# Performance work log

Hardware: AMD Instinct MI355X
Metric: run time of the kernel (lower is better)

The kernel has to match this reference:

```python
import jax, jax.numpy as jnp
import numpy as np

L, K, C, D, E = 4, 3, 512, 512, 512   # layers, kwidth, channels, embed_dim, encoding_dim
T, B, S, V, MAXT = 1024, 16, 512, 32, 1024


def setup_inputs() -> dict:
    key = jax.random.key(0)
    ks = jax.random.split(key, 16)
    n = lambda k, sh, s=0.02: jax.random.normal(k, sh, dtype=jnp.float32) * s
    return {
        "labels": jax.random.randint(ks[0], (T, B), 0, V),
        "enc_seq": jax.random.uniform(ks[1], (S, B, E), dtype=jnp.float32),
        "label_embed_W": n(ks[2], (V, D)),
        "time_embed_W": n(ks[3], (MAXT, D)),
        "conv_glu_w": n(ks[4], (L, C, C, K)),
        "conv_glu_b": jnp.zeros((L, C), jnp.float32),
        "conv_id_w": n(ks[5], (L, C, C, K)),
        "conv_id_b": jnp.zeros((L, C), jnp.float32),
        "res_proj_w": n(ks[6], (L, C, C)),
        "res_proj_b": jnp.zeros((L, C), jnp.float32),
        "inres_w": n(ks[7], (L, C, D)),
        "inres_b": jnp.zeros((L, C), jnp.float32),
        "in2enc_w": n(ks[8], (L, E, C)),
        "in2enc_b": jnp.ones((L, E), jnp.float32),  # positive bias keeps sum-normalizer well conditioned
        "lab2enc_w": n(ks[9], (L, E, D)),
        "lab2enc_b": jnp.zeros((L, E), jnp.float32),
        "enc2in_w": n(ks[10], (L, C, E)),
        "enc2in_b": jnp.zeros((L, C), jnp.float32),
        "out_res_w": n(ks[11], (V, D)),
        "out_res_b": jnp.zeros((V,), jnp.float32),
        "out_proj_w": n(ks[12], (V, C)),
        "out_proj_b": jnp.zeros((V,), jnp.float32),
    }


def causal_conv(x, w, b):
    # x: (T, B, Cin); w: (Cout, Cin, K) -> left-padded (causal) conv, out (T, B, Cout)
    x_ = jnp.transpose(x, (1, 2, 0))  # (B, Cin, T)
    y = jax.lax.conv_general_dilated(
        x_, w, window_strides=(1,), padding=[(w.shape[-1] - 1, 0)],
        dimension_numbers=("NCH", "OIH", "NCH"))
    return jnp.transpose(y, (2, 0, 1)) + b


def reference(labels, enc_seq, label_embed_W, time_embed_W, conv_glu_w, conv_glu_b,
              conv_id_w, conv_id_b, res_proj_w, res_proj_b, inres_w, inres_b,
              in2enc_w, in2enc_b, lab2enc_w, lab2enc_b, enc2in_w, enc2in_b,
              out_res_w, out_res_b, out_proj_w, out_proj_b):
    Tn = labels.shape[0]
    emb = label_embed_W[labels] + time_embed_W[jnp.arange(Tn)][:, None, :]  # (T,B,D)
    h = emb
    for i in range(conv_glu_w.shape[0]):
        x = causal_conv(h, conv_glu_w[i], conv_glu_b[i])
        g = causal_conv(h, conv_id_w[i], conv_id_b[i])
        conv_out = (x * jax.nn.sigmoid(g)
                    + jnp.einsum('tbc,oc->tbo', h, res_proj_w[i]) + res_proj_b[i])
        # attention: dot-product scores normalized by their SUM over encoder axis (no softmax)
        d = (jnp.einsum('tbc,ec->tbe', conv_out, in2enc_w[i]) + in2enc_b[i]
             + jnp.einsum('tbd,ed->tbe', emb, lab2enc_w[i]) + lab2enc_b[i])
        raw = jnp.einsum('tbe,sbe->tsb', d, enc_seq)          # (T,S,B)
        attn = raw / jnp.sum(raw, axis=1, keepdims=True)
        ctx = jnp.einsum('tsb,sbe->tbe', attn, enc_seq)        # (T,B,E)
        ctx_proj = jnp.einsum('tbe,ce->tbc', ctx, enc2in_w[i]) + enc2in_b[i]
        h = conv_out + ctx_proj + jnp.einsum('tbd,cd->tbc', emb, inres_w[i]) + inres_b[i]
    out = (jnp.einsum('tbc,vc->tbv', h, out_proj_w) + out_proj_b
           + jnp.einsum('tbd,vd->tbv', emb, out_res_w) + out_res_b)
    return out
```

## Files before the change

### kernel.cpp

```cpp
#include <hip/hip_runtime.h>
#include <math.h>

#define Tn 1024
#define Bn 16
#define Sn 512
#define Vn 32
#define Cn 512
#define En 512
#define Ln 4
#define Kw 3
#define MROWS 16384
#define PADROWS 32
#define PADE (PADROWS * Cn)

typedef short bf16x8 __attribute__((ext_vector_type(8)));
typedef float f32x4 __attribute__((ext_vector_type(4)));

__device__ __forceinline__ unsigned short cvt_bf16(float x) {
  unsigned u = __builtin_bit_cast(unsigned, x);
  u = (u + 0x7FFFu + ((u >> 16) & 1u)) >> 16;
  return (unsigned short)u;
}
__device__ __forceinline__ float bf2f(unsigned short h) {
  unsigned u = ((unsigned)h) << 16;
  return __builtin_bit_cast(float, u);
}

#define GL16(g, l)                                                                     \
  __builtin_amdgcn_global_load_lds((const __attribute__((address_space(1))) void*)(g), \
                                   (__attribute__((address_space(3))) void*)(l), 16, 0, 0)

template <int N>
__device__ __forceinline__ void wait_vm_bar() {
  asm volatile("s_waitcnt vmcnt(%0)\n\ts_barrier" ::"i"(N) : "memory");
}
__device__ __forceinline__ void tail_bar() {
  asm volatile("s_waitcnt lgkmcnt(0)\n\ts_barrier" ::: "memory");
}

__device__ __forceinline__ const unsigned short* seg_sel(const unsigned short* s0,
                                                         const unsigned short* s1,
                                                         const unsigned short* s2, int q) {
  const unsigned short* r = s0;
  r = (q == 1) ? s1 : r;
  r = (q == 2) ? s2 : r;
  return r;
}

template <int EPI, int NKT>
__global__ __launch_bounds__(512, 4) void g2(
    const unsigned short* __restrict__ a0, const unsigned short* __restrict__ a1,
    const unsigned short* __restrict__ a2, int ald, size_t az,
    const unsigned short* __restrict__ b0, const unsigned short* __restrict__ b1,
    const unsigned short* __restrict__ b2, int bld, size_t bz,
    const float* __restrict__ bias, const unsigned short* __restrict__ addbf,
    const float* __restrict__ dden, unsigned short* __restrict__ out, int old_, size_t oz) {
  __shared__ char SA[32768], SB[32768];
  const int tid = threadIdx.x;
  const int lane = tid & 63, wave = tid >> 6;
  const int r15 = lane & 15;
  const int sq = ((lane >> 4) ^ ((r15 >> 1) & 3)) << 4;
  const int waveM = (wave >> 2) << 6;
  const int waveN = (wave & 3) << 5;
  const int m0 = blockIdx.x * 128, n0 = blockIdx.y * 128;
  const int z = blockIdx.z;
  const unsigned short* A0 = a0 + (size_t)z * az;
  const unsigned short* A1 = a1 + (size_t)z * az;
  const unsigned short* A2 = a2 + (size_t)z * az;
  const unsigned short* B0 = b0 + (size_t)z * bz;
  const unsigned short* B1 = b1 + (size_t)z * bz;
  const unsigned short* B2 = b2 + (size_t)z * bz;
  const int strow = tid >> 2;
  const int stcol = ((tid & 3) ^ ((tid >> 3) & 3)) << 3;
  const int lofs = tid * 16;
  f32x4 acc[4][2] = {};

#define STAGE_T(KT, SL)                                                                  \
  do {                                                                                   \
    const unsigned short* ab_ = seg_sel(A0, A1, A2, (KT) >> 3) +                         \
                                (size_t)(m0 + strow) * ald + (((KT) & 7) << 6) + stcol;  \
    const unsigned short* bb_ = seg_sel(B0, B1, B2, (KT) >> 3) +                         \
                                (size_t)(n0 + strow) * bld + (((KT) & 7) << 6) + stcol;  \
    GL16(ab_, SA + (SL) * 16384 + lofs);                                                 \
    GL16(ab_ + 32, SA + (SL) * 16384 + 8192 + lofs);                                     \
    GL16(bb_, SB + (SL) * 16384 + lofs);                                                 \
    GL16(bb_ + 32, SB + (SL) * 16384 + 8192 + lofs);                                     \
  } while (0)

  STAGE_T(0, 0);
  for (int kt = 0; kt < NKT; ++kt) {
    const int sl = kt & 1;
    if (kt + 1 < NKT) {
      STAGE_T(kt + 1, sl ^ 1);
      wait_vm_bar<4>();
    } else {
      wait_vm_bar<0>();
    }
    const char* abase = SA + sl * 16384 + (waveM + r15) * 64 + sq;
    const char* bbase = SB + sl * 16384 + (waveN + r15) * 64 + sq;
    __builtin_amdgcn_s_setprio(1);
#pragma unroll
    for (int kp = 0; kp < 2; ++kp) {
      bf16x8 af[4], bfv[2];
#pragma unroll
      for (int i = 0; i < 4; ++i) af[i] = *(const bf16x8*)(abase + kp * 8192 + i * 1024);
#pragma unroll
      for (int j = 0; j < 2; ++j) bfv[j] = *(const bf16x8*)(bbase + kp * 8192 + j * 1024);
#pragma unroll
      for (int i = 0; i < 4; ++i)
#pragma unroll
        for (int j = 0; j < 2; ++j)
          acc[i][j] = __builtin_amdgcn_mfma_f32_16x16x32_bf16(af[i], bfv[j], acc[i][j], 0, 0, 0);
    }
    __builtin_amdgcn_s_setprio(0);
    tail_bar();
  }
#undef STAGE_T

  const int q4 = (lane >> 4) << 2;
#pragma unroll
  for (int i = 0; i < 4; ++i) {
    int row = m0 + waveM + i * 16 + q4;
    if constexpr (EPI == 0) {
      int xcol = ((n0 + waveN) >> 1) + r15;
      float bx = bias[n0 + waveN + r15];
      float bg = bias[n0 + waveN + 16 + r15];
#pragma unroll
      for (int rr = 0; rr < 4; ++rr) {
        float xv = acc[i][0][rr] + bx;
        float gv = acc[i][1][rr] + bg;
        float sg = 1.f / (1.f + __expf(-gv));
        out[(size_t)(row + rr) * 512 + xcol] = cvt_bf16(xv * sg);
      }
    } else if constexpr (EPI == 3) {
#pragma unroll
      for (int rr = 0; rr < 4; ++rr) {
        float inv = 1.f / dden[z + (size_t)(row + rr) * 16];
#pragma unroll
        for (int j = 0; j < 2; ++j) {
          int col = n0 + waveN + j * 16 + r15;
          out[(size_t)z * oz + (size_t)(row + rr) * old_ + col] = cvt_bf16(acc[i][j][rr] * inv);
        }
      }
    } else {
#pragma unroll
      for (int j = 0; j < 2; ++j) {
        int col = n0 + waveN + j * 16 + r15;
        float bb = (EPI == 4) ? 0.f : bias[col];
#pragma unroll
        for (int rr = 0; rr < 4; ++rr) {
          size_t o = (size_t)z * oz + (size_t)(row + rr) * old_ + col;
          float v = acc[i][j][rr] + bb;
          if constexpr (EPI == 2) v += bf2f(addbf[o]);
          out[o] = cvt_bf16(v);
        }
      }
    }
  }
}

__global__ __launch_bounds__(256, 4) void k_outm(const unsigned short* __restrict__ hd,
                                                 const unsigned short* __restrict__ embd,
                                                 const unsigned short* __restrict__ wcat2,
                                                 const float* __restrict__ bcat2,
                                                 float* __restrict__ out) {
  __shared__ char SA[32768];
  __shared__ char SBo[8192];
  const int tid = threadIdx.x;
  const int lane = tid & 63, wave = tid >> 6;
  const int r15 = lane & 15;
  const int sq = ((lane >> 4) ^ ((r15 >> 1) & 3)) << 4;
  const int waveM = wave << 5;
  const int m0 = blockIdx.x * 128;
  f32x4 acc[2][2] = {};
  const int aru = ((tid & 255) + 0);
  (void)aru;

#define OSTAGE(KT, SL)                                                                         \
  do {                                                                                         \
    const unsigned short* aseg = ((KT) < 8) ? hd : embd;                                       \
    int kc = ((KT) & 7) << 6;                                                                  \
    _Pragma("unroll") for (int q = 0; q < 2; ++q) {                                            \
      int unit = q * 256 + tid;                                                                \
      int row = unit >> 2, chunk = unit & 3;                                                   \
      int swc = chunk ^ ((row >> 1) & 3);                                                      \
      GL16(aseg + (size_t)(m0 + row) * 512 + kc + swc * 8, SA + (SL) * 16384 + unit * 16);     \
      GL16(aseg + (size_t)(m0 + row) * 512 + kc + 32 + swc * 8,                                \
           SA + (SL) * 16384 + 8192 + unit * 16);                                              \
    }                                                                                          \
    {                                                                                          \
      int half = tid >> 7;                                                                     \
      int u = tid & 127;                                                                       \
      int row = u >> 2, chunk = u & 3;                                                         \
      int swc = chunk ^ ((row >> 1) & 3);                                                      \
      GL16(wcat2 + (size_t)row * 1024 + ((KT) << 6) + half * 32 + swc * 8,                     \
           SBo + (SL) * 4096 + half * 2048 + u * 16);                                          \
    }                                                                                          \
  } while (0)

  OSTAGE(0, 0);
  for (int kt = 0; kt < 16; ++kt) {
    const int sl = kt & 1;
    if (kt + 1 < 16) {
      OSTAGE(kt + 1, sl ^ 1);
      wait_vm_bar<5>();
    } else {
      wait_vm_bar<0>();
    }
    const char* abase = SA + sl * 16384 + (waveM + r15) * 64 + sq;
    const char* bbase = SBo + sl * 4096 + r15 * 64 + sq;
    __builtin_amdgcn_s_setprio(1);
#pragma unroll
    for (int kp = 0; kp < 2; ++kp) {
      bf16x8 af[2], bfv[2];
#pragma unroll
      for (int i = 0; i < 2; ++i) af[i] = *(const bf16x8*)(abase + kp * 8192 + i * 1024);
#pragma unroll
      for (int j = 0; j < 2; ++j) bfv[j] = *(const bf16x8*)(bbase + kp * 2048 + j * 1024);
#pragma unroll
      for (int i = 0; i < 2; ++i)
#pragma unroll
        for (int j = 0; j < 2; ++j)
          acc[i][j] = __builtin_amdgcn_mfma_f32_16x16x32_bf16(af[i], bfv[j], acc[i][j], 0, 0, 0);
    }
    __builtin_amdgcn_s_setprio(0);
    tail_bar();
  }
#undef OSTAGE

  const int q4 = (lane >> 4) << 2;
#pragma unroll
  for (int i = 0; i < 2; ++i) {
    int row = m0 + waveM + i * 16 + q4;
#pragma unroll
    for (int j = 0; j < 2; ++j) {
      int col = j * 16 + r15;
      float bb = bcat2[col];
#pragma unroll
      for (int rr = 0; rr < 4; ++rr)
        out[(size_t)(row + rr) * 32 + col] = acc[i][j][rr] + bb;
    }
  }
}


__global__ __launch_bounds__(256) void emb_kernel(const int* __restrict__ labels,
                                                  const float* __restrict__ labW,
                                                  const float* __restrict__ timeW,
                                                  unsigned short* __restrict__ embd) {
  int idx = blockIdx.x * 256 + threadIdx.x;
  int dd = idx & 511;
  int m = idx >> 9;
  int t = m >> 4;
  embd[idx] = cvt_bf16(labW[labels[m] * 512 + dd] + timeW[t * 512 + dd]);
}

__global__ void k_zeropad(unsigned short* a, unsigned short* b, unsigned short* c) {
  int i = blockIdx.x * 256 + threadIdx.x;
  a[i] = 0; b[i] = 0; c[i] = 0;
}

__global__ void k_wcat(const float* __restrict__ wx, const float* __restrict__ wg,
                       unsigned short* __restrict__ wcat) {
  int idx = blockIdx.x * 256 + threadIdx.x;
  int k = idx % 1536;
  int tmp = idx / 1536;
  int orow = tmp & 1023;
  int l = tmp >> 10;
  int tap = k >> 9, c = k & 511;
  int q = orow >> 5, r = orow & 31;
  int srow = q * 16 + (r & 15);
  const float* src = (r < 16) ? wx : wg;
  float v = src[(((size_t)l * 512 + srow) * 512 + c) * 3 + tap];
  wcat[idx] = cvt_bf16(v);
}

__global__ void k_biascat(const float* __restrict__ bx, const float* __restrict__ bg,
                          float* __restrict__ bcat) {
  int idx = blockIdx.x * 256 + threadIdx.x;
  int orow = idx & 1023, l = idx >> 10;
  int q = orow >> 5, r = orow & 31;
  bcat[idx] = (r < 16) ? bx[l * 512 + q * 16 + r] : bg[l * 512 + q * 16 + (r & 15)];
}

__global__ void k_wcat2(const float* __restrict__ opw, const float* __restrict__ orw,
                        const float* __restrict__ opb, const float* __restrict__ orb,
                        unsigned short* __restrict__ wcat2, float* __restrict__ bcat2) {
  int idx = blockIdx.x * 256 + threadIdx.x;
  int v = idx >> 10, k = idx & 1023;
  float val = (k < 512) ? opw[v * 512 + k] : orw[v * 512 + k - 512];
  wcat2[idx] = cvt_bf16(val);
  if (idx < 32) bcat2[idx] = opb[idx] + orb[idx];
}

__global__ void cast_kernel(const float* __restrict__ src, unsigned short* __restrict__ dst,
                            int n) {
  int i = blockIdx.x * 256 + threadIdx.x;
  if (i < n) dst[i] = cvt_bf16(src[i]);
}

__global__ __launch_bounds__(256) void k_tr512(const float* __restrict__ w,
                                               unsigned short* __restrict__ wt) {
  __shared__ unsigned short t[64][65];
  int r0 = blockIdx.x * 64, c0 = blockIdx.y * 64;
  size_t base = (size_t)blockIdx.z * 512 * 512;
  int c = threadIdx.x & 63, rr = threadIdx.x >> 6;
#pragma unroll
  for (int i = 0; i < 16; ++i) {
    int r = rr + i * 4;
    t[r][c] = cvt_bf16(w[base + (size_t)(r0 + r) * 512 + c0 + c]);
  }
  __syncthreads();
#pragma unroll
  for (int i = 0; i < 16; ++i) {
    int r = rr + i * 4;
    wt[base + (size_t)(c0 + r) * 512 + r0 + c] = t[c][r];
  }
}

__global__ void esum_kernel(const float* __restrict__ enc, float* __restrict__ Esum) {
  int p = blockIdx.x * 256 + threadIdx.x;
  float s = 0.f;
  for (int ss = 0; ss < Sn; ++ss) s += enc[(size_t)ss * Bn * En + p];
  Esum[p] = s;
}

__global__ __launch_bounds__(256) void k_encT(const float* __restrict__ enc,
                                              unsigned short* __restrict__ encT) {
  __shared__ unsigned short t[64][66];
  int s0 = blockIdx.x * 64, e0 = blockIdx.y * 64, b = blockIdx.z;
  int c = threadIdx.x & 63, r0 = threadIdx.x >> 6;
#pragma unroll
  for (int i = 0; i < 16; ++i) {
    int r = r0 + i * 4;
    t[r][c] = cvt_bf16(enc[((size_t)(s0 + r) * Bn + b) * En + e0 + c]);
  }
  __syncthreads();
#pragma unroll
  for (int i = 0; i < 16; ++i) {
    int r = r0 + i * 4;
    encT[((size_t)b * En + e0 + r) * Sn + s0 + c] = t[c][r];
  }
}

__global__ void k_biasprep(const float* __restrict__ i2e, const float* __restrict__ res_b,
                           const float* __restrict__ in2enc_b, const float* __restrict__ lab2enc_b,
                           const float* __restrict__ e2i_b, const float* __restrict__ inres_b,
                           float* __restrict__ bd, float* __restrict__ bh) {
  int idx = blockIdx.x * 256 + threadIdx.x;
  int l = idx >> 9;
  float v = 0.f;
  const float* row = i2e + (size_t)idx * 512;
  const float* rb = res_b + l * 512;
  for (int c = 0; c < 512; ++c) v += row[c] * rb[c];
  bd[idx] = v + in2enc_b[idx] + lab2enc_b[idx];
  bh[idx] = res_b[idx] + e2i_b[idx] + inres_b[idx];
}

__global__ __launch_bounds__(256) void den_kernel(const unsigned short* __restrict__ d,
                                                  const float* __restrict__ Esum,
                                                  float* __restrict__ den) {
  int gtid = blockIdx.x * 256 + threadIdx.x;
  int row = gtid >> 6;
  int lane = threadIdx.x & 63;
  int b = row & 15;
  const unsigned short* dp = d + (size_t)row * 512 + lane * 8;
  const float* ep = Esum + b * 512 + lane * 8;
  float s = 0.f;
#pragma unroll
  for (int q = 0; q < 8; ++q) s += bf2f(dp[q]) * ep[q];
  for (int off = 32; off; off >>= 1) s += __shfl_down(s, off, 64);
  if (lane == 0) den[row] = s;
}


extern "C" void kernel_launch(void* const* d_in, const int* in_sizes, int n_in,
                              void* d_out, int out_size, void* d_ws, size_t ws_size,
                              hipStream_t stream) {
  const int* labels = (const int*)d_in[0];
  const float* enc = (const float*)d_in[1];
  const float* labW = (const float*)d_in[2];
  const float* timeW = (const float*)d_in[3];
  const float* conv_glu_w = (const float*)d_in[4];
  const float* conv_glu_b = (const float*)d_in[5];
  const float* conv_id_w = (const float*)d_in[6];
  const float* conv_id_b = (const float*)d_in[7];
  const float* res_proj_w = (const float*)d_in[8];
  const float* res_proj_b = (const float*)d_in[9];
  const float* inres_w = (const float*)d_in[10];
  const float* inres_b = (const float*)d_in[11];
  const float* in2enc_w = (const float*)d_in[12];
  const float* in2enc_b = (const float*)d_in[13];
  const float* lab2enc_w = (const float*)d_in[14];
  const float* lab2enc_b = (const float*)d_in[15];
  const float* enc2in_w = (const float*)d_in[16];
  const float* enc2in_b = (const float*)d_in[17];
  const float* out_res_w = (const float*)d_in[18];
  const float* out_res_b = (const float*)d_in[19];
  const float* out_proj_w = (const float*)d_in[20];
  const float* out_proj_b = (const float*)d_in[21];
  float* out = (float*)d_out;

  char* cur = (char*)d_ws;
  auto alloc = [&](size_t bytes) {
    char* p = cur;
    cur += (bytes + 255) & ~(size_t)255;
    return p;
  };
  const size_t BIG = (size_t)MROWS * 512;
  const size_t WN = (size_t)Ln * Cn * Cn;
  const size_t ZL = (size_t)512 * 512;
  float* den = (float*)alloc(MROWS * 4);
  float* EsumB = (float*)alloc(Bn * En * 4);
  float* bd = (float*)alloc(Ln * 512 * 4);
  float* bh = (float*)alloc(Ln * 512 * 4);
  float* bcat = (float*)alloc(Ln * 1024 * 4);
  float* bcat2 = (float*)alloc(32 * 4);
  unsigned short* embp = (unsigned short*)alloc((PADE + BIG) * 2);
  unsigned short* h0p = (unsigned short*)alloc((PADE + BIG) * 2);
  unsigned short* h1p = (unsigned short*)alloc((PADE + BIG) * 2);
  unsigned short* glubf = (unsigned short*)alloc(BIG * 2);
  unsigned short* dbf = (unsigned short*)alloc(BIG * 2);
  unsigned short* ctxbf = (unsigned short*)alloc(BIG * 2);
  unsigned short* encT = (unsigned short*)alloc((size_t)Bn * En * Sn * 2);
  unsigned short* Mbf = (unsigned short*)alloc((size_t)Bn * En * En * 2);
  unsigned short* wres = (unsigned short*)alloc(WN * 2);
  unsigned short* resT = (unsigned short*)alloc(WN * 2);
  unsigned short* wfuse = (unsigned short*)alloc(WN * 2);
  unsigned short* wcat = (unsigned short*)alloc((size_t)Ln * 1024 * 1536 * 2);
  unsigned short* wcat2 = (unsigned short*)alloc((size_t)32 * 1024 * 2);
  unsigned short* w_i2e = (unsigned short*)alloc(WN * 2);
  unsigned short* w_l2e = (unsigned short*)alloc(WN * 2);
  unsigned short* w_inr = (unsigned short*)alloc(WN * 2);
  unsigned short* w_e2i = (unsigned short*)alloc(WN * 2);

  unsigned short* embd = embp + PADE;
  unsigned short* h0d = h0p + PADE;
  unsigned short* h1d = h1p + PADE;

  emb_kernel<<<MROWS * 512 / 256, 256, 0, stream>>>(labels, labW, timeW, embd);
  k_zeropad<<<PADE / 256, 256, 0, stream>>>(embp, h0p, h1p);
  k_wcat<<<Ln * 1024 * 1536 / 256, 256, 0, stream>>>(conv_glu_w, conv_id_w, wcat);
  k_biascat<<<Ln * 1024 / 256, 256, 0, stream>>>(conv_glu_b, conv_id_b, bcat);
  k_wcat2<<<32 * 1024 / 256, 256, 0, stream>>>(out_proj_w, out_res_w, out_proj_b, out_res_b,
                                               wcat2, bcat2);
  cast_kernel<<<WN / 256, 256, 0, stream>>>(res_proj_w, wres, WN);
  cast_kernel<<<WN / 256, 256, 0, stream>>>(in2enc_w, w_i2e, WN);
  cast_kernel<<<WN / 256, 256, 0, stream>>>(lab2enc_w, w_l2e, WN);
  cast_kernel<<<WN / 256, 256, 0, stream>>>(inres_w, w_inr, WN);
  cast_kernel<<<WN / 256, 256, 0, stream>>>(enc2in_w, w_e2i, WN);
  k_tr512<<<dim3(8, 8, Ln), 256, 0, stream>>>(res_proj_w, resT);
  k_biasprep<<<Ln * 512 / 256, 256, 0, stream>>>(in2enc_w, res_proj_b, in2enc_b, lab2enc_b,
                                                 enc2in_b, inres_b, bd, bh);
  esum_kernel<<<Bn * En / 256, 256, 0, stream>>>(enc, EsumB);
  k_encT<<<dim3(Sn / 64, En / 64, Bn), 256, 0, stream>>>(enc, encT);
  g2<4, 8><<<dim3(4, 4, Bn), 512, 0, stream>>>(encT, encT, encT, Sn, ZL, encT, encT, encT, Sn,
                                               ZL, nullptr, nullptr, nullptr, Mbf, 512, ZL);
  g2<4, 8><<<dim3(4, 4, Ln), 512, 0, stream>>>(w_i2e, w_i2e, w_i2e, 512, ZL, resT, resT, resT,
                                               512, ZL, nullptr, nullptr, nullptr, wfuse, 512, ZL);

  const unsigned short* hdata = embd;
  unsigned short* hbufs[2] = {h0d, h1d};
  for (int l = 0; l < Ln; ++l) {
    const size_t wo = (size_t)l * Cn * Cn;
    const unsigned short* wc = wcat + (size_t)l * 1024 * 1536;
    g2<0, 24><<<dim3(128, 8), 512, 0, stream>>>(
        hdata - 2 * Bn * 512, hdata - Bn * 512, hdata, 512, 0, wc, wc + 512, wc + 1024, 1536, 0,
        bcat + l * 1024, nullptr, nullptr, glubf, 512, 0);
    g2<1, 24><<<dim3(128, 4), 512, 0, stream>>>(
        glubf, hdata, embd, 512, 0, w_i2e + wo, wfuse + wo, w_l2e + wo, 512, 0, bd + l * 512,
        nullptr, nullptr, dbf, 512, 0);
    den_kernel<<<MROWS / 4, 256, 0, stream>>>(dbf, EsumB, den);
    g2<3, 8><<<dim3(8, 4, Bn), 512, 0, stream>>>(dbf, dbf, dbf, 8192, 512, Mbf, Mbf, Mbf, 512,
                                                 ZL, nullptr, nullptr, den, ctxbf, 8192, 512);
    g2<2, 24><<<dim3(128, 4), 512, 0, stream>>>(
        hdata, ctxbf, embd, 512, 0, wres + wo, w_e2i + wo, w_inr + wo, 512, 0, bh + l * 512,
        glubf, nullptr, hbufs[l & 1], 512, 0);
    hdata = hbufs[l & 1];
  }

  k_outm<<<MROWS / 128, 256, 0, stream>>>(hdata, embd, wcat2, bcat2, out);
}
```

Measured before the change: 669.4 us.

## Add 256x128-tile GEMM kernel with fused denominator partials; merge prep kernels

Adds a new GEMM kernel g3t with 256x128 tiles, split A/B staging waits and 4x4 MFMA accumulators per wave. It replaces the N=512 GEMMs for the attention query d and the residual h update. The d GEMM now computes per-row partial dot products with Esum in its epilogue, so the separate den_kernel pass that re-read dbf is replaced by a small k_densum plus a precomputed bias term (k_bden). The many small prep kernels (embedding, zero padding, weight casts and concatenation) are merged into two launches to cut launch overhead. The trade-off is more registers and lower occupancy (launch bounds of 2 blocks), plus an extra den8 buffer, and the denominator is now computed from the fp32 accumulators rather than from the rounded bf16 dbf.

Result: slower. 699.4 us (+4.5%).

```diff
diff --git a/kernel.cpp b/kernel.cpp
--- a/kernel.cpp
+++ b/kernel.cpp
@@ -37,6 +37,11 @@
 __device__ __forceinline__ void tail_bar() {
   asm volatile("s_waitcnt lgkmcnt(0)\n\ts_barrier" ::: "memory");
 }
+#define VMB(N)                                               \
+  do {                                                       \
+    asm volatile("s_waitcnt vmcnt(%0)" ::"i"(N) : "memory"); \
+    __builtin_amdgcn_s_barrier();                            \
+  } while (0)
 
 __device__ __forceinline__ const unsigned short* seg_sel(const unsigned short* s0,
                                                          const unsigned short* s1,
@@ -53,8 +58,8 @@
     const unsigned short* __restrict__ a2, int ald, size_t az,
     const unsigned short* __restrict__ b0, const unsigned short* __restrict__ b1,
     const unsigned short* __restrict__ b2, int bld, size_t bz,
-    const float* __restrict__ bias, const unsigned short* __restrict__ addbf,
-    const float* __restrict__ dden, unsigned short* __restrict__ out, int old_, size_t oz) {
+    const float* __restrict__ bias, const float* __restrict__ dden,
+    unsigned short* __restrict__ out, int old_, size_t oz) {
   __shared__ char SA[32768], SB[32768];
   const int tid = threadIdx.x;
   const int lane = tid & 63, wave = tid >> 6;
@@ -75,16 +80,16 @@
   const int lofs = tid * 16;
   f32x4 acc[4][2] = {};
 
-#define STAGE_T(KT, SL)                                                                  \
-  do {                                                                                   \
-    const unsigned short* ab_ = seg_sel(A0, A1, A2, (KT) >> 3) +                         \
-                                (size_t)(m0 + strow) * ald + (((KT) & 7) << 6) + stcol;  \
-    const unsigned short* bb_ = seg_sel(B0, B1, B2, (KT) >> 3) +                         \
-                                (size_t)(n0 + strow) * bld + (((KT) & 7) << 6) + stcol;  \
-    GL16(ab_, SA + (SL) * 16384 + lofs);                                                 \
-    GL16(ab_ + 32, SA + (SL) * 16384 + 8192 + lofs);                                     \
-    GL16(bb_, SB + (SL) * 16384 + lofs);                                                 \
-    GL16(bb_ + 32, SB + (SL) * 16384 + 8192 + lofs);                                     \
+#define STAGE_T(KT, SL)                                                               \
+  do {                                                                                \
+    const unsigned short* ab_ = seg_sel(A0, A1, A2, (KT) >> 3) +                      \
+                                (size_t)(m0 + strow) * ald + (((KT)&7) << 6) + stcol; \
+    const unsigned short* bb_ = seg_sel(B0, B1, B2, (KT) >> 3) +                      \
+                                (size_t)(n0 + strow) * bld + (((KT)&7) << 6) + stcol; \
+    GL16(ab_, SA + (SL)*16384 + lofs);                                                \
+    GL16(ab_ + 32, SA + (SL)*16384 + 8192 + lofs);                                    \
+    GL16(bb_, SB + (SL)*16384 + lofs);                                                \
+    GL16(bb_ + 32, SB + (SL)*16384 + 8192 + lofs);                                    \
   } while (0)
 
   STAGE_T(0, 0);
@@ -150,13 +155,156 @@
 #pragma unroll
         for (int rr = 0; rr < 4; ++rr) {
           size_t o = (size_t)z * oz + (size_t)(row + rr) * old_ + col;
-          float v = acc[i][j][rr] + bb;
-          if constexpr (EPI == 2) v += bf2f(addbf[o]);
-          out[o] = cvt_bf16(v);
+          out[o] = cvt_bf16(acc[i][j][rr] + bb);
         }
       }
     }
   }
+}
+
+template <int EPI>
+__global__ __launch_bounds__(512, 2) void g3t(
+    const unsigned short* __restrict__ a0, const unsigned short* __restrict__ a1,
+    const unsigned short* __restrict__ a2, const unsigned short* __restrict__ b0,
+    const unsigned short* __restrict__ b1, const unsigned short* __restrict__ b2,
+    const float* __restrict__ bias, const unsigned short* __restrict__ addbf,
+    const float* __restrict__ Esum, float* __restrict__ den8,
+    unsigned short* __restrict__ out) {
+  __shared__ char LA[2][32768];
+  __shared__ char LB[2][16384];
+  const int tid = threadIdx.x;
+  const int lane = tid & 63;
+  const int wm = (tid >> 6) >> 1;
+  const int wn = (tid >> 6) & 1;
+  const int r15 = lane & 15;
+  const int l4 = lane >> 4;
+  const int q4 = l4 << 2;
+  const int m0 = blockIdx.x * 256, n0 = blockIdx.y * 128;
+  const int srow = tid >> 3;
+  const int scol = (((tid & 7) ^ (srow & 7)) << 3);
+  const int sdst = tid << 4;
+  f32x4 acc[4][4] = {};
+  bf16x8 afr[4][2], b01[2][2], b23[2][2];
+
+#define TGA(KT, BB)                                                              \
+  do {                                                                           \
+    const unsigned short* s_ = seg_sel(a0, a1, a2, (KT) >> 3) +                  \
+                               (size_t)(m0 + srow) * 512 + (((KT)&7) << 6) + scol; \
+    GL16(s_, LA[BB] + sdst);                                                     \
+    GL16(s_ + (size_t)64 * 512, LA[BB] + 8192 + sdst);                           \
+    GL16(s_ + (size_t)128 * 512, LA[BB] + 16384 + sdst);                         \
+    GL16(s_ + (size_t)192 * 512, LA[BB] + 24576 + sdst);                         \
+  } while (0)
+#define TGB(KT, BB)                                                              \
+  do {                                                                           \
+    const unsigned short* s_ = seg_sel(b0, b1, b2, (KT) >> 3) +                  \
+                               (size_t)(n0 + srow) * 512 + (((KT)&7) << 6) + scol; \
+    GL16(s_, LB[BB] + sdst);                                                     \
+    GL16(s_ + (size_t)64 * 512, LB[BB] + 8192 + sdst);                           \
+  } while (0)
+#define TRA(SL)                                                                            \
+  do {                                                                                     \
+    _Pragma("unroll") for (int f = 0; f < 4; ++f) _Pragma("unroll") for (int kp = 0;       \
+                                                                         kp < 2; ++kp) {  \
+      int ar = ((f >> 1) << 7) + (wm << 5) + ((f & 1) << 4) + r15;                         \
+      afr[f][kp] =                                                                         \
+          *(const bf16x8*)(LA[SL] + ar * 128 + ((((kp << 2) | l4) ^ (ar & 7)) << 4));      \
+    }                                                                                      \
+  } while (0)
+#define TRB(SL, CH, DST)                                                                   \
+  do {                                                                                     \
+    _Pragma("unroll") for (int c = 0; c < 2; ++c) _Pragma("unroll") for (int kp = 0;       \
+                                                                         kp < 2; ++kp) {  \
+      int br = ((CH) << 6) + (wn << 5) + (c << 4) + r15;                                   \
+      DST[c][kp] =                                                                         \
+          *(const bf16x8*)(LB[SL] + br * 128 + ((((kp << 2) | l4) ^ (br & 7)) << 4));      \
+    }                                                                                      \
+  } while (0)
+#define MMT(BF, C0)                                                                        \
+  do {                                                                                     \
+    __builtin_amdgcn_s_setprio(1);                                                         \
+    _Pragma("unroll") for (int f = 0; f < 4; ++f) _Pragma("unroll") for (int c = 0; c < 2; \
+                                                                         ++c)             \
+        _Pragma("unroll") for (int kp = 0; kp < 2; ++kp) acc[f][(C0) + c] =                \
+            __builtin_amdgcn_mfma_f32_16x16x32_bf16(afr[f][kp], BF[c][kp],                 \
+                                                    acc[f][(C0) + c], 0, 0, 0);            \
+    __builtin_amdgcn_s_setprio(0);                                                         \
+  } while (0)
+#define TGRP(KT, W1, W2, STG)                       \
+  do {                                              \
+    const int sl_ = (KT)&1, sn_ = sl_ ^ 1;          \
+    if (STG) TGA((KT) + 1, sn_);                    \
+    VMB(W1);                                        \
+    TRA(sl_);                                       \
+    TRB(sl_, 0, b01);                               \
+    MMT(b01, 0);                                    \
+    if (STG) TGB((KT) + 1, sn_);                    \
+    VMB(W2);                                        \
+    TRB(sl_, 1, b23);                               \
+    MMT(b23, 2);                                    \
+  } while (0)
+
+  TGA(0, 0);
+  TGB(0, 0);
+  for (int kt = 0; kt < 23; ++kt) TGRP(kt, 5, 6, 1);
+  TGRP(23, 1, 0, 0);
+#undef TGRP
+
+#pragma unroll
+  for (int f = 0; f < 4; ++f) {
+    int grow = m0 + ((f >> 1) << 7) + (wm << 5) + ((f & 1) << 4) + q4;
+#pragma unroll
+    for (int c = 0; c < 4; ++c) {
+      int gcol = n0 + ((c >> 1) << 6) + (wn << 5) + ((c & 1) << 4) + r15;
+      float bb = bias[gcol];
+#pragma unroll
+      for (int rr = 0; rr < 4; ++rr) {
+        size_t o = (size_t)(grow + rr) * 512 + gcol;
+        float v = acc[f][c][rr] + bb;
+        if constexpr (EPI == 2) v += bf2f(addbf[o]);
+        out[o] = cvt_bf16(v);
+      }
+    }
+  }
+  if constexpr (EPI == 1) {
+#pragma unroll
+    for (int f = 0; f < 4; ++f) {
+#pragma unroll
+      for (int rr = 0; rr < 4; ++rr) {
+        int row = m0 + ((f >> 1) << 7) + (wm << 5) + ((f & 1) << 4) + q4 + rr;
+        int b = row & 15;
+        float s = 0.f;
+#pragma unroll
+        for (int c = 0; c < 4; ++c) {
+          int gcol = n0 + ((c >> 1) << 6) + (wn << 5) + ((c & 1) << 4) + r15;
+          s += acc[f][c][rr] * Esum[b * 512 + gcol];
+        }
+        s += __shfl_xor(s, 1, 64);
+        s += __shfl_xor(s, 2, 64);
+        s += __shfl_xor(s, 4, 64);
+        s += __shfl_xor(s, 8, 64);
+        if (r15 == 0) den8[(size_t)(blockIdx.y * 2 + wn) * MROWS + row] = s;
+      }
+    }
+  }
+}
+
+__global__ void k_densum(const float* __restrict__ den8, const float* __restrict__ bdenl,
+                         float* __restrict__ den) {
+  int row = blockIdx.x * 256 + threadIdx.x;
+  float s = bdenl[row & 15];
+#pragma unroll
+  for (int q = 0; q < 8; ++q) s += den8[(size_t)q * MROWS + row];
+  den[row] = s;
+}
+
+__global__ void k_bden(const float* __restrict__ bd, const float* __restrict__ Esum,
+                       float* __restrict__ bden) {
+  int idx = threadIdx.x;
+  int l = idx >> 4, b = idx & 15;
+  float s = 0.f;
+  for (int c = 0; c < 512; ++c) s += bd[l * 512 + c] * Esum[b * 512 + c];
+  bden[idx] = s;
 }
 
 __global__ __launch_bounds__(256, 4) void k_outm(const unsigned short* __restrict__ hd,
@@ -173,29 +321,27 @@
   const int waveM = wave << 5;
   const int m0 = blockIdx.x * 128;
   f32x4 acc[2][2] = {};
-  const int aru = ((tid & 255) + 0);
-  (void)aru;
-
-#define OSTAGE(KT, SL)                                                                         \
-  do {                                                                                         \
-    const unsigned short* aseg = ((KT) < 8) ? hd : embd;                                       \
-    int kc = ((KT) & 7) << 6;                                                                  \
-    _Pragma("unroll") for (int q = 0; q < 2; ++q) {                                            \
-      int unit = q * 256 + tid;                                                                \
-      int row = unit >> 2, chunk = unit & 3;                                                   \
-      int swc = chunk ^ ((row >> 1) & 3);                                                      \
-      GL16(aseg + (size_t)(m0 + row) * 512 + kc + swc * 8, SA + (SL) * 16384 + unit * 16);     \
-      GL16(aseg + (size_t)(m0 + row) * 512 + kc + 32 + swc * 8,                                \
-           SA + (SL) * 16384 + 8192 + unit * 16);                                              \
-    }                                                                                          \
-    {                                                                                          \
-      int half = tid >> 7;                                                                     \
-      int u = tid & 127;                                                                       \
-      int row = u >> 2, chunk = u & 3;                                                         \
-      int swc = chunk ^ ((row >> 1) & 3);                                                      \
-      GL16(wcat2 + (size_t)row * 1024 + ((KT) << 6) + half * 32 + swc * 8,                     \
-           SBo + (SL) * 4096 + half * 2048 + u * 16);                                          \
-    }                                                                                          \
+
+#define OSTAGE(KT, SL)                                                                   \
+  do {                                                                                   \
+    const unsigned short* aseg = ((KT) < 8) ? hd : embd;                                 \
+    int kc = ((KT)&7) << 6;                                                              \
+    _Pragma("unroll") for (int q = 0; q < 2; ++q) {                                      \
+      int unit = q * 256 + tid;                                                          \
+      int row = unit >> 2, chunk = unit & 3;                                             \
+      int swc = chunk ^ ((row >> 1) & 3);                                                \
+      GL16(aseg + (size_t)(m0 + row) * 512 + kc + swc * 8, SA + (SL)*16384 + unit * 16); \
+      GL16(aseg + (size_t)(m0 + row) * 512 + kc + 32 + swc * 8,                          \
+           SA + (SL)*16384 + 8192 + unit * 16);                                          \
+    }                                                                                    \
+    {                                                                                    \
+      int half = tid >> 7;                                                               \
+      int u = tid & 127;                                                                 \
+      int row = u >> 2, chunk = u & 3;                                                   \
+      int swc = chunk ^ ((row >> 1) & 3);                                                \
+      GL16(wcat2 + (size_t)row * 1024 + ((KT) << 6) + half * 32 + swc * 8,               \
+           SBo + (SL)*4096 + half * 2048 + u * 16);                                      \
+    }                                                                                    \
   } while (0)
 
   OSTAGE(0, 0);
@@ -237,66 +383,88 @@
       int col = j * 16 + r15;
       float bb = bcat2[col];
 #pragma unroll
-      for (int rr = 0; rr < 4; ++rr)
-        out[(size_t)(row + rr) * 32 + col] = acc[i][j][rr] + bb;
-    }
-  }
-}
-
-
-__global__ __launch_bounds__(256) void emb_kernel(const int* __restrict__ labels,
-                                                  const float* __restrict__ labW,
-                                                  const float* __restrict__ timeW,
-                                                  unsigned short* __restrict__ embd) {
+      for (int rr = 0; rr < 4; ++rr) out[(size_t)(row + rr) * 32 + col] = acc[i][j][rr] + bb;
+    }
+  }
+}
+
+
+__global__ __launch_bounds__(256) void k_prep2(const int* __restrict__ labels,
+                                               const float* __restrict__ labW,
+                                               const float* __restrict__ timeW,
+                                               unsigned short* __restrict__ embd,
+                                               unsigned short* __restrict__ embp,
+                                               unsigned short* __restrict__ h0p,
+                                               unsigned short* __restrict__ h1p) {
   int idx = blockIdx.x * 256 + threadIdx.x;
-  int dd = idx & 511;
-  int m = idx >> 9;
-  int t = m >> 4;
-  embd[idx] = cvt_bf16(labW[labels[m] * 512 + dd] + timeW[t * 512 + dd]);
-}
-
-__global__ void k_zeropad(unsigned short* a, unsigned short* b, unsigned short* c) {
-  int i = blockIdx.x * 256 + threadIdx.x;
-  a[i] = 0; b[i] = 0; c[i] = 0;
-}
-
-__global__ void k_wcat(const float* __restrict__ wx, const float* __restrict__ wg,
-                       unsigned short* __restrict__ wcat) {
+  if (idx < MROWS * 512) {
+    int dd = idx & 511;
+    int m = idx >> 9;
+    int t = m >> 4;
+    embd[idx] = cvt_bf16(labW[labels[m] * 512 + dd] + timeW[t * 512 + dd]);
+    return;
+  }
+  int i = idx - MROWS * 512;
+  if (i < PADE) embp[i] = 0;
+  else if (i < 2 * PADE) h0p[i - PADE] = 0;
+  else h1p[i - 2 * PADE] = 0;
+}
+
+__global__ __launch_bounds__(256) void k_prep1(
+    const float* __restrict__ res_proj_w, const float* __restrict__ in2enc_w,
+    const float* __restrict__ lab2enc_w, const float* __restrict__ inres_w,
+    const float* __restrict__ enc2in_w, const float* __restrict__ wx,
+    const float* __restrict__ wg, const float* __restrict__ cbx, const float* __restrict__ cbg,
+    const float* __restrict__ opw, const float* __restrict__ orw, const float* __restrict__ opb,
+    const float* __restrict__ orb, unsigned short* __restrict__ wres,
+    unsigned short* __restrict__ w_i2e, unsigned short* __restrict__ w_l2e,
+    unsigned short* __restrict__ w_inr, unsigned short* __restrict__ w_e2i,
+    unsigned short* __restrict__ wcat, float* __restrict__ bcat,
+    unsigned short* __restrict__ wcat2, float* __restrict__ bcat2) {
   int idx = blockIdx.x * 256 + threadIdx.x;
-  int k = idx % 1536;
-  int tmp = idx / 1536;
-  int orow = tmp & 1023;
-  int l = tmp >> 10;
-  int tap = k >> 9, c = k & 511;
-  int q = orow >> 5, r = orow & 31;
-  int srow = q * 16 + (r & 15);
-  const float* src = (r < 16) ? wx : wg;
-  float v = src[(((size_t)l * 512 + srow) * 512 + c) * 3 + tap];
-  wcat[idx] = cvt_bf16(v);
-}
-
-__global__ void k_biascat(const float* __restrict__ bx, const float* __restrict__ bg,
-                          float* __restrict__ bcat) {
-  int idx = blockIdx.x * 256 + threadIdx.x;
-  int orow = idx & 1023, l = idx >> 10;
-  int q = orow >> 5, r = orow & 31;
-  bcat[idx] = (r < 16) ? bx[l * 512 + q * 16 + r] : bg[l * 512 + q * 16 + (r & 15)];
-}
-
-__global__ void k_wcat2(const float* __restrict__ opw, const float* __restrict__ orw,
-                        const float* __restrict__ opb, const float* __restrict__ orb,
-                        unsigned short* __restrict__ wcat2, float* __restrict__ bcat2) {
-  int idx = blockIdx.x * 256 + threadIdx.x;
-  int v = idx >> 10, k = idx & 1023;
-  float val = (k < 512) ? opw[v * 512 + k] : orw[v * 512 + k - 512];
-  wcat2[idx] = cvt_bf16(val);
-  if (idx < 32) bcat2[idx] = opb[idx] + orb[idx];
-}
-
-__global__ void cast_kernel(const float* __restrict__ src, unsigned short* __restrict__ dst,
-                            int n) {
-  int i = blockIdx.x * 256 + threadIdx.x;
-  if (i < n) dst[i] = cvt_bf16(src[i]);
+  const int WNc = 1 << 20;
+  if (idx < 5 * WNc) {
+    int which = idx >> 20, i = idx & (WNc - 1);
+    const float* s = (which == 0)   ? res_proj_w
+                     : (which == 1) ? in2enc_w
+                     : (which == 2) ? lab2enc_w
+                     : (which == 3) ? inres_w
+                                    : enc2in_w;
+    unsigned short* d = (which == 0)   ? wres
+                        : (which == 1) ? w_i2e
+                        : (which == 2) ? w_l2e
+                        : (which == 3) ? w_inr
+                                       : w_e2i;
+    d[i] = cvt_bf16(s[i]);
+    return;
+  }
+  idx -= 5 * WNc;
+  if (idx < Ln * 1024 * 1536) {
+    int k = idx % 1536;
+    int tmp = idx / 1536;
+    int orow = tmp & 1023;
+    int l = tmp >> 10;
+    int tap = k >> 9, c = k & 511;
+    int q = orow >> 5, r = orow & 31;
+    int srow = q * 16 + (r & 15);
+    const float* src = (r < 16) ? wx : wg;
+    wcat[idx] = cvt_bf16(src[(((size_t)l * 512 + srow) * 512 + c) * 3 + tap]);
+    return;
+  }
+  idx -= Ln * 1024 * 1536;
+  if (idx < Ln * 1024) {
+    int orow = idx & 1023, l = idx >> 10;
+    int q = orow >> 5, r = orow & 31;
+    bcat[idx] = (r < 16) ? cbx[l * 512 + q * 16 + r] : cbg[l * 512 + q * 16 + (r & 15)];
+    return;
+  }
+  idx -= Ln * 1024;
+  {
+    int v = idx >> 10, k = idx & 1023;
+    float val = (k < 512) ? opw[v * 512 + k] : orw[v * 512 + k - 512];
+    wcat2[idx] = cvt_bf16(val);
+    if (idx < 32) bcat2[idx] = opb[idx] + orb[idx];
+  }
 }
 
 __global__ __launch_bounds__(256) void k_tr512(const float* __restrict__ w,
@@ -355,22 +523,6 @@
   for (int c = 0; c < 512; ++c) v += row[c] * rb[c];
   bd[idx] = v + in2enc_b[idx] + lab2enc_b[idx];
   bh[idx] = res_b[idx] + e2i_b[idx] + inres_b[idx];
-}
-
-__global__ __launch_bounds__(256) void den_kernel(const unsigned short* __restrict__ d,
-                                                  const float* __restrict__ Esum,
-                                                  float* __restrict__ den) {
-  int gtid = blockIdx.x * 256 + threadIdx.x;
-  int row = gtid >> 6;
-  int lane = threadIdx.x & 63;
-  int b = row & 15;
-  const unsigned short* dp = d + (size_t)row * 512 + lane * 8;
-  const float* ep = Esum + b * 512 + lane * 8;
-  float s = 0.f;
-#pragma unroll
-  for (int q = 0; q < 8; ++q) s += bf2f(dp[q]) * ep[q];
-  for (int off = 32; off; off >>= 1) s += __shfl_down(s, off, 64);
-  if (lane == 0) den[row] = s;
 }
 
 
@@ -411,6 +563,8 @@
   const size_t WN = (size_t)Ln * Cn * Cn;
   const size_t ZL = (size_t)512 * 512;
   float* den = (float*)alloc(MROWS * 4);
+  float* den8 = (float*)alloc((size_t)8 * MROWS * 4);
+  float* bden = (float*)alloc(Ln * Bn * 4);
   float* EsumB = (float*)alloc(Bn * En * 4);
   float* bd = (float*)alloc(Ln * 512 * 4);
   float* bh = (float*)alloc(Ln * 512 * 4);
@@ -438,44 +592,43 @@
   unsigned short* h0d = h0p + PADE;
   unsigned short* h1d = h1p + PADE;
 
-  emb_kernel<<<MROWS * 512 / 256, 256, 0, stream>>>(labels, labW, timeW, embd);
-  k_zeropad<<<PADE / 256, 256, 0, stream>>>(embp, h0p, h1p);
-  k_wcat<<<Ln * 1024 * 1536 / 256, 256, 0, stream>>>(conv_glu_w, conv_id_w, wcat);
-  k_biascat<<<Ln * 1024 / 256, 256, 0, stream>>>(conv_glu_b, conv_id_b, bcat);
-  k_wcat2<<<32 * 1024 / 256, 256, 0, stream>>>(out_proj_w, out_res_w, out_proj_b, out_res_b,
-                                               wcat2, bcat2);
-  cast_kernel<<<WN / 256, 256, 0, stream>>>(res_proj_w, wres, WN);
-  cast_kernel<<<WN / 256, 256, 0, stream>>>(in2enc_w, w_i2e, WN);
-  cast_kernel<<<WN / 256, 256, 0, stream>>>(lab2enc_w, w_l2e, WN);
-  cast_kernel<<<WN / 256, 256, 0, stream>>>(inres_w, w_inr, WN);
-  cast_kernel<<<WN / 256, 256, 0, stream>>>(enc2in_w, w_e2i, WN);
+  k_prep2<<<(MROWS * 512 + 3 * PADE) / 256, 256, 0, stream>>>(labels, labW, timeW, embd, embp,
+                                                              h0p, h1p);
+  {
+    int total = 5 * (1 << 20) + Ln * 1024 * 1536 + Ln * 1024 + 32 * 1024;
+    k_prep1<<<total / 256, 256, 0, stream>>>(res_proj_w, in2enc_w, lab2enc_w, inres_w, enc2in_w,
+                                             conv_glu_w, conv_id_w, conv_glu_b, conv_id_b,
+                                             out_proj_w, out_res_w, out_proj_b, out_res_b, wres,
+                                             w_i2e, w_l2e, w_inr, w_e2i, wcat, bcat, wcat2,
+                                             bcat2);
+  }
   k_tr512<<<dim3(8, 8, Ln), 256, 0, stream>>>(res_proj_w, resT);
+  esum_kernel<<<Bn * En / 256, 256, 0, stream>>>(enc, EsumB);
   k_biasprep<<<Ln * 512 / 256, 256, 0, stream>>>(in2enc_w, res_proj_b, in2enc_b, lab2enc_b,
                                                  enc2in_b, inres_b, bd, bh);
-  esum_kernel<<<Bn * En / 256, 256, 0, stream>>>(enc, EsumB);
+  k_bden<<<1, Ln * Bn, 0, stream>>>(bd, EsumB, bden);
   k_encT<<<dim3(Sn / 64, En / 64, Bn), 256, 0, stream>>>(enc, encT);
   g2<4, 8><<<dim3(4, 4, Bn), 512, 0, stream>>>(encT, encT, encT, Sn, ZL, encT, encT, encT, Sn,
-                                               ZL, nullptr, nullptr, nullptr, Mbf, 512, ZL);
+                                               ZL, nullptr, nullptr, Mbf, 512, ZL);
   g2<4, 8><<<dim3(4, 4, Ln), 512, 0, stream>>>(w_i2e, w_i2e, w_i2e, 512, ZL, resT, resT, resT,
-                                               512, ZL, nullptr, nullptr, nullptr, wfuse, 512, ZL);
+                                               512, ZL, nullptr, nullptr, wfuse, 512, ZL);
 
   const unsigned short* hdata = embd;
   unsigned short* hbufs[2] = {h0d, h1d};
   for (int l = 0; l < Ln; ++l) {
     const size_t wo = (size_t)l * Cn * Cn;
     const unsigned short* wc = wcat + (size_t)l * 1024 * 1536;
-    g2<0, 24><<<dim3(128, 8), 512, 0, stream>>>(
-        hdata - 2 * Bn * 512, hdata - Bn * 512, hdata, 512, 0, wc, wc + 512, wc + 1024, 1536, 0,
-        bcat + l * 1024, nullptr, nullptr, glubf, 512, 0);
-    g2<1, 24><<<dim3(128, 4), 512, 0, stream>>>(
-        glubf, hdata, embd, 512, 0, w_i2e + wo, wfuse + wo, w_l2e + wo, 512, 0, bd + l * 512,
-        nullptr, nullptr, dbf, 512, 0);
-    den_kernel<<<MROWS / 4, 256, 0, stream>>>(dbf, EsumB, den);
+    g2<0, 24><<<dim3(128, 8), 512, 0, stream>>>(hdata - 2 * Bn * 512, hdata - Bn * 512, hdata,
+                                                512, 0, wc, wc + 512, wc + 1024, 1536, 0,
+                                                bcat + l * 1024, nullptr, glubf, 512, 0);
+    g3t<1><<<dim3(64, 4), 512, 0, stream>>>(glubf, hdata, embd, w_i2e + wo, wfuse + wo,
+                                            w_l2e + wo, bd + l * 512, nullptr, EsumB, den8, dbf);
+    k_densum<<<MROWS / 256, 256, 0, stream>>>(den8, bden + l * Bn, den);
     g2<3, 8><<<dim3(8, 4, Bn), 512, 0, stream>>>(dbf, dbf, dbf, 8192, 512, Mbf, Mbf, Mbf, 512,
-                                                 ZL, nullptr, nullptr, den, ctxbf, 8192, 512);
-    g2<2, 24><<<dim3(128, 4), 512, 0, stream>>>(
-        hdata, ctxbf, embd, 512, 0, wres + wo, w_e2i + wo, w_inr + wo, 512, 0, bh + l * 512,
-        glubf, nullptr, hbufs[l & 1], 512, 0);
+                                                 ZL, nullptr, den, ctxbf, 8192, 512);
+    g3t<2><<<dim3(64, 4), 512, 0, stream>>>(hdata, ctxbf, embd, wres + wo, w_e2i + wo,
+                                            w_inr + wo, bh + l * 512, glubf, nullptr, nullptr,
+                                            hbufs[l & 1]);
     hdata = hbufs[l & 1];
   }
 
```
